# Kernel tuning notes

Measured on AMD Instinct MI355X. Metric: run time of the kernel, lower is better.

Reference implementation:

```python
import jax, jax.numpy as jnp
import numpy as np

N, M = 50000, 16
NODE_DIM, EDGE_DIM = 128, 64
CONCAT_DIM = 2 * NODE_DIM + EDGE_DIM  # 320
LN_EPS = 1e-6  # flax.linen.LayerNorm default


def setup_inputs() -> dict:
    key = jax.random.key(0)
    ks = jax.random.split(key, 5)
    x = jax.random.normal(ks[0], (N, NODE_DIM), dtype=jnp.float32)
    nbr_fea = jax.random.normal(ks[1], (N, M, EDGE_DIM), dtype=jnp.float32)
    nbr_fea_idx = jax.random.randint(ks[2], (N, M), 0, N)
    ln_scale = jnp.ones((NODE_DIM,), dtype=jnp.float32)
    ln_bias = jnp.zeros((NODE_DIM,), dtype=jnp.float32)
    # lecun_normal-ish init scaled by fan-in (flax Dense default is lecun_normal)
    W1 = jax.random.normal(ks[3], (CONCAT_DIM, NODE_DIM), dtype=jnp.float32) / np.sqrt(CONCAT_DIM)
    b1 = jnp.zeros((NODE_DIM,), dtype=jnp.float32)
    W2 = jax.random.normal(ks[4], (NODE_DIM, NODE_DIM), dtype=jnp.float32) / np.sqrt(NODE_DIM)
    b2 = jnp.zeros((NODE_DIM,), dtype=jnp.float32)
    return {"x": x, "nbr_fea": nbr_fea, "nbr_fea_idx": nbr_fea_idx,
            "ln_scale": ln_scale, "ln_bias": ln_bias,
            "W1": W1, "b1": b1, "W2": W2, "b2": b2}


def _layer_norm(x, scale, bias):
    mu = jnp.mean(x, axis=-1, keepdims=True)
    var = jnp.mean(jnp.square(x - mu), axis=-1, keepdims=True)
    return (x - mu) * jax.lax.rsqrt(var + LN_EPS) * scale + bias


def reference(x, nbr_fea, nbr_fea_idx, ln_scale, ln_bias, W1, b1, W2, b2):
    # x: [N, D], nbr_fea: [N, M, E], nbr_fea_idx: [N, M]
    x_normed = _layer_norm(x, ln_scale, ln_bias)                 # [N, D]
    x_nbr = jnp.take(x_normed, nbr_fea_idx, axis=0)              # [N, M, D]
    m = nbr_fea_idx.shape[1]
    x_center = jnp.broadcast_to(x_normed[:, None, :], (x.shape[0], m, x.shape[1]))
    concat = jnp.concatenate([x_center, x_nbr, nbr_fea], axis=-1)  # [N, M, 2D+E]
    h = jax.nn.silu(jnp.einsum('nmc,cd->nmd', concat, W1) + b1)   # [N, M, D]
    msg = jnp.einsum('nmd,de->nme', h, W2) + b2                   # [N, M, D]
    agg = jnp.sum(msg, axis=1)                                    # [N, D]
    return x + agg
```

## Files before the change

kernel.cpp:

```cpp
#include <hip/hip_runtime.h>
#include <math.h>

#define N_NODES 50000
#define M_NBR 16
#define D 128
#define E 64

typedef __attribute__((ext_vector_type(8))) __bf16 bf16x8;
typedef __attribute__((ext_vector_type(4))) float f32x4;

__device__ __forceinline__ void gload16(const void* g, void* l) {
  __builtin_amdgcn_global_load_lds(
      (const __attribute__((address_space(1))) void*)g,
      (__attribute__((address_space(3))) void*)l, 16, 0, 0);
}

__device__ __forceinline__ int swz(int o) { return o ^ (((o >> 7) & 7) << 4); }


__global__ __launch_bounds__(256) void k_prep(const float* __restrict__ W1,
                                              const float* __restrict__ W2,
                                              __bf16* __restrict__ w1a_f,
                                              __bf16* __restrict__ w1b_f,
                                              __bf16* __restrict__ w1c_f,
                                              __bf16* __restrict__ w2_f) {
  const int t = blockIdx.x * 256 + threadIdx.x;
  if (t < 16384) {
    const int j = t & 7, r = (t >> 3) & 15, c = (t >> 7) & 3, q = t >> 9;
    const int kt = q & 3, dt = q >> 2;
    w1a_f[t] = (__bf16)W1[(kt * 32 + c * 8 + j) * 128 + dt * 16 + r];
  } else if (t < 32768) {
    const int u = t - 16384;
    const int j = u & 7, r = (u >> 3) & 15, c = (u >> 7) & 3, q = u >> 9;
    const int kt = q & 3, dt = q >> 2;
    w1b_f[u] = (__bf16)W1[(128 + kt * 32 + c * 8 + j) * 128 + dt * 16 + r];
  } else if (t < 40960) {
    const int u = t - 32768;
    const int j = u & 7, r = (u >> 3) & 15, c = (u >> 7) & 3, q = u >> 9;
    const int kt = q & 1, dt = q >> 1;
    w1c_f[u] = (__bf16)W1[(256 + kt * 32 + c * 8 + j) * 128 + dt * 16 + r];
  } else if (t < 57344) {
    const int u = t - 40960;
    const int j = u & 7, r = (u >> 3) & 15, c = (u >> 7) & 3, q = u >> 9;
    const int kt = q & 3, dt = q >> 2;
    const int i = kt * 32 + c * 8 + j;
    const int ak = (i & 7) * 16 + (i >> 3);
    w2_f[u] = (__bf16)W2[ak * 128 + dt * 16 + r];
  }
}

__global__ __launch_bounds__(256) void k_t12f(const float* __restrict__ x,
                                              const float* __restrict__ sc,
                                              const float* __restrict__ bi,
                                              const __bf16* __restrict__ w1a_f,
                                              const __bf16* __restrict__ w1b_f,
                                              const float* __restrict__ b1,
                                              __bf16* __restrict__ t1bp,
                                              __bf16* __restrict__ t2bp) {
  const int wave = blockIdx.x * 4 + (threadIdx.x >> 6);
  if (wave >= N_NODES / 16) return;
  const int lane = threadIdx.x & 63;
  const int r = lane & 15, c = lane >> 4;
  const int node0 = wave * 16;

  const float* row = x + (size_t)(node0 + r) * 128 + c * 8;
  f32x4 va[8];
  #pragma unroll
  for (int kt = 0; kt < 4; ++kt) {
    va[2 * kt]     = *(const f32x4*)(row + kt * 32);
    va[2 * kt + 1] = *(const f32x4*)(row + kt * 32 + 4);
  }
  float s = 0.f;
  #pragma unroll
  for (int q = 0; q < 8; ++q) s += va[q][0] + va[q][1] + va[q][2] + va[q][3];
  s += __shfl_xor(s, 16, 64);
  s += __shfl_xor(s, 32, 64);
  const float mu = s * (1.0f / 128.0f);
  float qs = 0.f;
  #pragma unroll
  for (int q = 0; q < 8; ++q) {
    #pragma unroll
    for (int e = 0; e < 4; ++e) { const float dxx = va[q][e] - mu; qs += dxx * dxx; }
  }
  qs += __shfl_xor(qs, 16, 64);
  qs += __shfl_xor(qs, 32, 64);
  const float rs = rsqrtf(qs * (1.0f / 128.0f) + 1e-6f);

  bf16x8 af[4];
  #pragma unroll
  for (int kt = 0; kt < 4; ++kt) {
    const f32x4 s_lo = *(const f32x4*)(sc + kt * 32 + c * 8);
    const f32x4 s_hi = *(const f32x4*)(sc + kt * 32 + c * 8 + 4);
    const f32x4 b_lo = *(const f32x4*)(bi + kt * 32 + c * 8);
    const f32x4 b_hi = *(const f32x4*)(bi + kt * 32 + c * 8 + 4);
    #pragma unroll
    for (int e = 0; e < 4; ++e) {
      af[kt][e]     = (__bf16)(((va[2 * kt][e]     - mu) * rs) * s_lo[e] + b_lo[e]);
      af[kt][4 + e] = (__bf16)(((va[2 * kt + 1][e] - mu) * rs) * s_hi[e] + b_hi[e]);
    }
  }

  const bf16x8* wa = (const bf16x8*)w1a_f;
  const bf16x8* wb = (const bf16x8*)w1b_f;
  f32x4 acc1[8], acc2[8];
  #pragma unroll
  for (int dt = 0; dt < 8; ++dt) { acc1[dt] = (f32x4){0,0,0,0}; acc2[dt] = (f32x4){0,0,0,0}; }
  #pragma unroll
  for (int dt = 0; dt < 8; ++dt) {
    #pragma unroll
    for (int kt = 0; kt < 4; ++kt) {
      const bf16x8 bfa = wa[(dt * 4 + kt) * 64 + c * 16 + r];
      acc1[dt] = __builtin_amdgcn_mfma_f32_16x16x32_bf16(af[kt], bfa, acc1[dt], 0, 0, 0);
      const bf16x8 bfb = wb[(dt * 4 + kt) * 64 + c * 16 + r];
      acc2[dt] = __builtin_amdgcn_mfma_f32_16x16x32_bf16(af[kt], bfb, acc2[dt], 0, 0, 0);
    }
  }

  float b1v[8];
  #pragma unroll
  for (int dt = 0; dt < 8; ++dt) b1v[dt] = b1[dt * 16 + r];
  #pragma unroll
  for (int j = 0; j < 4; ++j) {
    const int node = node0 + c * 4 + j;
    bf16x8 t1v, t2v;
    #pragma unroll
    for (int dt = 0; dt < 8; ++dt) {
      t1v[dt] = (__bf16)(acc1[dt][j] + b1v[dt]);
      t2v[dt] = (__bf16)acc2[dt][j];
    }
    *(bf16x8*)(t1bp + (size_t)node * 128 + r * 8) = t1v;
    *(bf16x8*)(t2bp + (size_t)node * 128 + r * 8) = t2v;
  }
}

__global__ __launch_bounds__(256, 4) void k_edge(const float* __restrict__ nbr,
                                                 const int* __restrict__ idx,
                                                 const __bf16* __restrict__ t1bp,
                                                 const __bf16* __restrict__ t2bp,
                                                 const __bf16* __restrict__ w1c_f,
                                                 __bf16* __restrict__ hsum_b) {
  __shared__ __bf16 wlds[8192];
  const int lane = threadIdx.x & 63;
  const int wid  = threadIdx.x >> 6;
  const int r = lane & 15, c = lane >> 4;

  {
    const int s0 = wid * 1024 + lane * 16;
    #pragma unroll
    for (int q = 0; q < 4; ++q) {
      const int s = s0 + q * 4096;
      gload16((const char*)w1c_f + swz(s), (char*)wlds + s);
    }
  }

  const int n = blockIdx.x * 4 + wid;
  const int4 g = *(const int4*)(idx + n * M_NBR + c * 4);
  const float* arow = nbr + (size_t)n * (M_NBR * E) + r * E + c * 8;
  const f32x4 a0 = *(const f32x4*)(arow);
  const f32x4 a1 = *(const f32x4*)(arow + 4);
  const f32x4 a2 = *(const f32x4*)(arow + 32);
  const f32x4 a3 = *(const f32x4*)(arow + 36);
  const bf16x8 t1v = *(const bf16x8*)(t1bp + (size_t)n * 128 + r * 8);

  __syncthreads();

  const bf16x8 tg0 = *(const bf16x8*)(t2bp + (size_t)g.x * 128 + r * 8);
  const bf16x8 tg1 = *(const bf16x8*)(t2bp + (size_t)g.y * 128 + r * 8);
  const bf16x8 tg2 = *(const bf16x8*)(t2bp + (size_t)g.z * 128 + r * 8);
  const bf16x8 tg3 = *(const bf16x8*)(t2bp + (size_t)g.w * 128 + r * 8);

  bf16x8 af0, af1;
  #pragma unroll
  for (int e = 0; e < 4; ++e) {
    af0[e] = (__bf16)a0[e]; af0[4 + e] = (__bf16)a1[e];
    af1[e] = (__bf16)a2[e]; af1[4 + e] = (__bf16)a3[e];
  }

  f32x4 acc[8];
  #pragma unroll
  for (int dt = 0; dt < 8; ++dt) acc[dt] = (f32x4){0, 0, 0, 0};
  #pragma unroll
  for (int dt = 0; dt < 8; ++dt) {
    const int o0 = ((dt * 2 + 0) * 64 + c * 16 + r) * 16;
    const int o1 = ((dt * 2 + 1) * 64 + c * 16 + r) * 16;
    const bf16x8 b0 = *(const bf16x8*)((const char*)wlds + swz(o0));
    const bf16x8 b1 = *(const bf16x8*)((const char*)wlds + swz(o1));
    acc[dt] = __builtin_amdgcn_mfma_f32_16x16x32_bf16(af0, b0, acc[dt], 0, 0, 0);
    acc[dt] = __builtin_amdgcn_mfma_f32_16x16x32_bf16(af1, b1, acc[dt], 0, 0, 0);
  }

  float ssum[8];
  #pragma unroll
  for (int dt = 0; dt < 8; ++dt) {
    const float tb = (float)t1v[dt];
    float s = 0.f;
    { const float h = acc[dt][0] + tb + (float)tg0[dt]; s += __fdividef(h, 1.0f + __expf(-h)); }
    { const float h = acc[dt][1] + tb + (float)tg1[dt]; s += __fdividef(h, 1.0f + __expf(-h)); }
    { const float h = acc[dt][2] + tb + (float)tg2[dt]; s += __fdividef(h, 1.0f + __expf(-h)); }
    { const float h = acc[dt][3] + tb + (float)tg3[dt]; s += __fdividef(h, 1.0f + __expf(-h)); }
    s += __shfl_xor(s, 16, 64);
    s += __shfl_xor(s, 32, 64);
    ssum[dt] = s;
  }
  if (lane < 16) {
    bf16x8 hs;
    #pragma unroll
    for (int dt = 0; dt < 8; ++dt) hs[dt] = (__bf16)ssum[dt];
    *(bf16x8*)(hsum_b + (size_t)n * 128 + r * 8) = hs;
  }
}

__global__ __launch_bounds__(256) void k_out(const __bf16* __restrict__ hsum_b,
                                             const __bf16* __restrict__ w2_f,
                                             const float* __restrict__ b2,
                                             const float* __restrict__ x,
                                             float* __restrict__ out) {
  const int wave = blockIdx.x * 4 + (threadIdx.x >> 6);
  if (wave >= N_NODES / 16) return;
  const int lane = threadIdx.x & 63;
  const int r = lane & 15, c = lane >> 4;
  const int node0 = wave * 16;

  const __bf16* row = hsum_b + (size_t)(node0 + r) * 128 + c * 8;
  bf16x8 af[4];
  #pragma unroll
  for (int kt = 0; kt < 4; ++kt) af[kt] = *(const bf16x8*)(row + kt * 32);

  const bf16x8* w2 = (const bf16x8*)w2_f;
  f32x4 acc[8];
  #pragma unroll
  for (int dt = 0; dt < 8; ++dt) acc[dt] = (f32x4){0,0,0,0};
  #pragma unroll
  for (int dt = 0; dt < 8; ++dt) {
    #pragma unroll
    for (int kt = 0; kt < 4; ++kt) {
      const bf16x8 bf = w2[(dt * 4 + kt) * 64 + c * 16 + r];
      acc[dt] = __builtin_amdgcn_mfma_f32_16x16x32_bf16(af[kt], bf, acc[dt], 0, 0, 0);
    }
  }

  float b2v[8];
  #pragma unroll
  for (int dt = 0; dt < 8; ++dt) b2v[dt] = 16.0f * b2[dt * 16 + r];
  #pragma unroll
  for (int j = 0; j < 4; ++j) {
    const int node = node0 + c * 4 + j;
    #pragma unroll
    for (int dt = 0; dt < 8; ++dt) {
      const size_t o = (size_t)node * 128 + dt * 16 + r;
      out[o] = x[o] + acc[dt][j] + b2v[dt];
    }
  }
}

extern "C" void kernel_launch(void* const* d_in, const int* in_sizes, int n_in,
                              void* d_out, int out_size, void* d_ws, size_t ws_size,
                              hipStream_t stream) {
  const float* x        = (const float*)d_in[0];
  const float* nbr_fea  = (const float*)d_in[1];
  const int*   nbr_idx  = (const int*)d_in[2];
  const float* ln_scale = (const float*)d_in[3];
  const float* ln_bias  = (const float*)d_in[4];
  const float* W1       = (const float*)d_in[5];
  const float* b1       = (const float*)d_in[6];
  const float* W2       = (const float*)d_in[7];
  const float* b2       = (const float*)d_in[8];
  float* out = (float*)d_out;

  char* ws = (char*)d_ws;
  __bf16* t1bp   = (__bf16*)(ws);
  __bf16* hsum_b = (__bf16*)(ws + 12800000);
  __bf16* t2bp   = (__bf16*)(ws + 25600000);
  __bf16* w1a_f  = (__bf16*)(ws + 38400000);
  __bf16* w1b_f  = (__bf16*)(ws + 38433536);
  __bf16* w1c_f  = (__bf16*)(ws + 38466304);
  __bf16* w2_f   = (__bf16*)(ws + 38482688);

  k_prep <<<224, 256, 0, stream>>>(W1, W2, w1a_f, w1b_f, w1c_f, w2_f);
  k_t12f <<<(N_NODES / 16 + 3) / 4, 256, 0, stream>>>(x, ln_scale, ln_bias,
                                                      w1a_f, w1b_f, b1, t1bp, t2bp);
  k_edge <<<N_NODES / 4, 256, 0, stream>>>(nbr_fea, nbr_idx, t1bp, t2bp, w1c_f, hsum_b);
  k_out  <<<(N_NODES / 16 + 3) / 4, 256, 0, stream>>>(hsum_b, w2_f, b2, x, out);
}
```

Measured before the change: 122.7 us.

## Fuse edge aggregation and output projection into one kernel via LDS staging

Merges the edge kernel and the W2 output kernel. Each block now handles 16 nodes, four per wave, and stages the bf16 per-node silu sums in padded LDS, then runs the W2 MFMA and the residual add in the same block. This removes the hsum round trip through global memory and one kernel launch. The W2 prep permutation is changed to a plain row order to match the new LDS layout. In exchange, blocks are 4x fewer and each wave processes its nodes serially, which may reduce latency hiding for the gathered loads.

Measured after the change: 120.0 us. -2.2%, faster.

```diff
diff --git a/kernel.cpp b/kernel.cpp
--- a/kernel.cpp
+++ b/kernel.cpp
@@ -43,9 +43,7 @@
     const int u = t - 40960;
     const int j = u & 7, r = (u >> 3) & 15, c = (u >> 7) & 3, q = u >> 9;
     const int kt = q & 3, dt = q >> 2;
-    const int i = kt * 32 + c * 8 + j;
-    const int ak = (i & 7) * 16 + (i >> 3);
-    w2_f[u] = (__bf16)W2[ak * 128 + dt * 16 + r];
+    w2_f[u] = (__bf16)W2[(kt * 32 + c * 8 + j) * 128 + dt * 16 + r];
   }
 }
 
@@ -133,16 +131,23 @@
   }
 }
 
-__global__ __launch_bounds__(256, 4) void k_edge(const float* __restrict__ nbr,
-                                                 const int* __restrict__ idx,
-                                                 const __bf16* __restrict__ t1bp,
-                                                 const __bf16* __restrict__ t2bp,
-                                                 const __bf16* __restrict__ w1c_f,
-                                                 __bf16* __restrict__ hsum_b) {
+#define HPITCH 136
+
+__global__ __launch_bounds__(256, 4) void k_edge2(const float* __restrict__ nbr,
+                                                  const int* __restrict__ idx,
+                                                  const __bf16* __restrict__ t1bp,
+                                                  const __bf16* __restrict__ t2bp,
+                                                  const __bf16* __restrict__ w1c_f,
+                                                  const __bf16* __restrict__ w2_f,
+                                                  const float* __restrict__ b2,
+                                                  const float* __restrict__ x,
+                                                  float* __restrict__ out) {
   __shared__ __bf16 wlds[8192];
+  __shared__ __bf16 hlds[16 * HPITCH];
   const int lane = threadIdx.x & 63;
   const int wid  = threadIdx.x >> 6;
   const int r = lane & 15, c = lane >> 4;
+  const int nb0 = blockIdx.x * 16;
 
   {
     const int s0 = wid * 1024 + lane * 16;
@@ -152,104 +157,89 @@
       gload16((const char*)w1c_f + swz(s), (char*)wlds + s);
     }
   }
-
-  const int n = blockIdx.x * 4 + wid;
-  const int4 g = *(const int4*)(idx + n * M_NBR + c * 4);
-  const float* arow = nbr + (size_t)n * (M_NBR * E) + r * E + c * 8;
-  const f32x4 a0 = *(const f32x4*)(arow);
-  const f32x4 a1 = *(const f32x4*)(arow + 4);
-  const f32x4 a2 = *(const f32x4*)(arow + 32);
-  const f32x4 a3 = *(const f32x4*)(arow + 36);
-  const bf16x8 t1v = *(const bf16x8*)(t1bp + (size_t)n * 128 + r * 8);
-
   __syncthreads();
 
-  const bf16x8 tg0 = *(const bf16x8*)(t2bp + (size_t)g.x * 128 + r * 8);
-  const bf16x8 tg1 = *(const bf16x8*)(t2bp + (size_t)g.y * 128 + r * 8);
-  const bf16x8 tg2 = *(const bf16x8*)(t2bp + (size_t)g.z * 128 + r * 8);
-  const bf16x8 tg3 = *(const bf16x8*)(t2bp + (size_t)g.w * 128 + r * 8);
-
-  bf16x8 af0, af1;
-  #pragma unroll
-  for (int e = 0; e < 4; ++e) {
-    af0[e] = (__bf16)a0[e]; af0[4 + e] = (__bf16)a1[e];
-    af1[e] = (__bf16)a2[e]; af1[4 + e] = (__bf16)a3[e];
-  }
-
-  f32x4 acc[8];
-  #pragma unroll
-  for (int dt = 0; dt < 8; ++dt) acc[dt] = (f32x4){0, 0, 0, 0};
-  #pragma unroll
-  for (int dt = 0; dt < 8; ++dt) {
-    const int o0 = ((dt * 2 + 0) * 64 + c * 16 + r) * 16;
-    const int o1 = ((dt * 2 + 1) * 64 + c * 16 + r) * 16;
-    const bf16x8 b0 = *(const bf16x8*)((const char*)wlds + swz(o0));
-    const bf16x8 b1 = *(const bf16x8*)((const char*)wlds + swz(o1));
-    acc[dt] = __builtin_amdgcn_mfma_f32_16x16x32_bf16(af0, b0, acc[dt], 0, 0, 0);
-    acc[dt] = __builtin_amdgcn_mfma_f32_16x16x32_bf16(af1, b1, acc[dt], 0, 0, 0);
-  }
-
-  float ssum[8];
-  #pragma unroll
-  for (int dt = 0; dt < 8; ++dt) {
-    const float tb = (float)t1v[dt];
-    float s = 0.f;
-    { const float h = acc[dt][0] + tb + (float)tg0[dt]; s += __fdividef(h, 1.0f + __expf(-h)); }
-    { const float h = acc[dt][1] + tb + (float)tg1[dt]; s += __fdividef(h, 1.0f + __expf(-h)); }
-    { const float h = acc[dt][2] + tb + (float)tg2[dt]; s += __fdividef(h, 1.0f + __expf(-h)); }
-    { const float h = acc[dt][3] + tb + (float)tg3[dt]; s += __fdividef(h, 1.0f + __expf(-h)); }
-    s += __shfl_xor(s, 16, 64);
-    s += __shfl_xor(s, 32, 64);
-    ssum[dt] = s;
-  }
-  if (lane < 16) {
-    bf16x8 hs;
-    #pragma unroll
-    for (int dt = 0; dt < 8; ++dt) hs[dt] = (__bf16)ssum[dt];
-    *(bf16x8*)(hsum_b + (size_t)n * 128 + r * 8) = hs;
-  }
-}
-
-__global__ __launch_bounds__(256) void k_out(const __bf16* __restrict__ hsum_b,
-                                             const __bf16* __restrict__ w2_f,
-                                             const float* __restrict__ b2,
-                                             const float* __restrict__ x,
-                                             float* __restrict__ out) {
-  const int wave = blockIdx.x * 4 + (threadIdx.x >> 6);
-  if (wave >= N_NODES / 16) return;
-  const int lane = threadIdx.x & 63;
-  const int r = lane & 15, c = lane >> 4;
-  const int node0 = wave * 16;
-
-  const __bf16* row = hsum_b + (size_t)(node0 + r) * 128 + c * 8;
-  bf16x8 af[4];
-  #pragma unroll
-  for (int kt = 0; kt < 4; ++kt) af[kt] = *(const bf16x8*)(row + kt * 32);
-
+  #pragma unroll
+  for (int i = 0; i < 4; ++i) {
+    const int row = wid * 4 + i;
+    const int n = nb0 + row;
+
+    const int4 g = *(const int4*)(idx + n * M_NBR + c * 4);
+    const float* arow = nbr + (size_t)n * (M_NBR * E) + r * E + c * 8;
+    const f32x4 a0 = *(const f32x4*)(arow);
+    const f32x4 a1 = *(const f32x4*)(arow + 4);
+    const f32x4 a2 = *(const f32x4*)(arow + 32);
+    const f32x4 a3 = *(const f32x4*)(arow + 36);
+    const bf16x8 t1v = *(const bf16x8*)(t1bp + (size_t)n * 128 + r * 8);
+    const bf16x8 tg0 = *(const bf16x8*)(t2bp + (size_t)g.x * 128 + r * 8);
+    const bf16x8 tg1 = *(const bf16x8*)(t2bp + (size_t)g.y * 128 + r * 8);
+    const bf16x8 tg2 = *(const bf16x8*)(t2bp + (size_t)g.z * 128 + r * 8);
+    const bf16x8 tg3 = *(const bf16x8*)(t2bp + (size_t)g.w * 128 + r * 8);
+
+    bf16x8 af0, af1;
+    #pragma unroll
+    for (int e = 0; e < 4; ++e) {
+      af0[e] = (__bf16)a0[e]; af0[4 + e] = (__bf16)a1[e];
+      af1[e] = (__bf16)a2[e]; af1[4 + e] = (__bf16)a3[e];
+    }
+
+    f32x4 acc[8];
+    #pragma unroll
+    for (int dt = 0; dt < 8; ++dt) acc[dt] = (f32x4){0, 0, 0, 0};
+    #pragma unroll
+    for (int dt = 0; dt < 8; ++dt) {
+      const int o0 = ((dt * 2 + 0) * 64 + c * 16 + r) * 16;
+      const int o1 = ((dt * 2 + 1) * 64 + c * 16 + r) * 16;
+      const bf16x8 b0 = *(const bf16x8*)((const char*)wlds + swz(o0));
+      const bf16x8 b1 = *(const bf16x8*)((const char*)wlds + swz(o1));
+      acc[dt] = __builtin_amdgcn_mfma_f32_16x16x32_bf16(af0, b0, acc[dt], 0, 0, 0);
+      acc[dt] = __builtin_amdgcn_mfma_f32_16x16x32_bf16(af1, b1, acc[dt], 0, 0, 0);
+    }
+
+    #pragma unroll
+    for (int dt = 0; dt < 8; ++dt) {
+      const float tb = (float)t1v[dt];
+      float s = 0.f;
+      { const float h = acc[dt][0] + tb + (float)tg0[dt]; s += __fdividef(h, 1.0f + __expf(-h)); }
+      { const float h = acc[dt][1] + tb + (float)tg1[dt]; s += __fdividef(h, 1.0f + __expf(-h)); }
+      { const float h = acc[dt][2] + tb + (float)tg2[dt]; s += __fdividef(h, 1.0f + __expf(-h)); }
+      { const float h = acc[dt][3] + tb + (float)tg3[dt]; s += __fdividef(h, 1.0f + __expf(-h)); }
+      s += __shfl_xor(s, 16, 64);
+      s += __shfl_xor(s, 32, 64);
+      if (lane < 16) hlds[row * HPITCH + dt * 16 + lane] = (__bf16)s;
+    }
+  }
+  __syncthreads();
+
+  const int dtA = wid * 2, dtB = wid * 2 + 1;
   const bf16x8* w2 = (const bf16x8*)w2_f;
-  f32x4 acc[8];
-  #pragma unroll
-  for (int dt = 0; dt < 8; ++dt) acc[dt] = (f32x4){0,0,0,0};
-  #pragma unroll
-  for (int dt = 0; dt < 8; ++dt) {
-    #pragma unroll
-    for (int kt = 0; kt < 4; ++kt) {
-      const bf16x8 bf = w2[(dt * 4 + kt) * 64 + c * 16 + r];
-      acc[dt] = __builtin_amdgcn_mfma_f32_16x16x32_bf16(af[kt], bf, acc[dt], 0, 0, 0);
-    }
-  }
-
-  float b2v[8];
-  #pragma unroll
-  for (int dt = 0; dt < 8; ++dt) b2v[dt] = 16.0f * b2[dt * 16 + r];
+  bf16x8 bA[4], bB[4];
+  #pragma unroll
+  for (int kt = 0; kt < 4; ++kt) {
+    bA[kt] = w2[(dtA * 4 + kt) * 64 + c * 16 + r];
+    bB[kt] = w2[(dtB * 4 + kt) * 64 + c * 16 + r];
+  }
+  bf16x8 haf[4];
+  #pragma unroll
+  for (int kt = 0; kt < 4; ++kt)
+    haf[kt] = *(const bf16x8*)(hlds + r * HPITCH + kt * 32 + c * 8);
+
+  f32x4 accA = (f32x4){0,0,0,0}, accB = (f32x4){0,0,0,0};
+  #pragma unroll
+  for (int kt = 0; kt < 4; ++kt) {
+    accA = __builtin_amdgcn_mfma_f32_16x16x32_bf16(haf[kt], bA[kt], accA, 0, 0, 0);
+    accB = __builtin_amdgcn_mfma_f32_16x16x32_bf16(haf[kt], bB[kt], accB, 0, 0, 0);
+  }
+
+  const float b2A = 16.0f * b2[dtA * 16 + r];
+  const float b2B = 16.0f * b2[dtB * 16 + r];
   #pragma unroll
   for (int j = 0; j < 4; ++j) {
-    const int node = node0 + c * 4 + j;
-    #pragma unroll
-    for (int dt = 0; dt < 8; ++dt) {
-      const size_t o = (size_t)node * 128 + dt * 16 + r;
-      out[o] = x[o] + acc[dt][j] + b2v[dt];
-    }
+    const int node = nb0 + c * 4 + j;
+    const size_t oA = (size_t)node * 128 + dtA * 16 + r;
+    const size_t oB = (size_t)node * 128 + dtB * 16 + r;
+    out[oA] = x[oA] + accA[j] + b2A;
+    out[oB] = x[oB] + accB[j] + b2B;
   }
 }
 
@@ -269,16 +259,15 @@
 
   char* ws = (char*)d_ws;
   __bf16* t1bp   = (__bf16*)(ws);
-  __bf16* hsum_b = (__bf16*)(ws + 12800000);
-  __bf16* t2bp   = (__bf16*)(ws + 25600000);
-  __bf16* w1a_f  = (__bf16*)(ws + 38400000);
-  __bf16* w1b_f  = (__bf16*)(ws + 38433536);
-  __bf16* w1c_f  = (__bf16*)(ws + 38466304);
-  __bf16* w2_f   = (__bf16*)(ws + 38482688);
-
-  k_prep <<<224, 256, 0, stream>>>(W1, W2, w1a_f, w1b_f, w1c_f, w2_f);
-  k_t12f <<<(N_NODES / 16 + 3) / 4, 256, 0, stream>>>(x, ln_scale, ln_bias,
-                                                      w1a_f, w1b_f, b1, t1bp, t2bp);
-  k_edge <<<N_NODES / 4, 256, 0, stream>>>(nbr_fea, nbr_idx, t1bp, t2bp, w1c_f, hsum_b);
-  k_out  <<<(N_NODES / 16 + 3) / 4, 256, 0, stream>>>(hsum_b, w2_f, b2, x, out);
-}
+  __bf16* t2bp   = (__bf16*)(ws + 12800000);
+  __bf16* w1a_f  = (__bf16*)(ws + 25600000);
+  __bf16* w1b_f  = (__bf16*)(ws + 25632768);
+  __bf16* w1c_f  = (__bf16*)(ws + 25665536);
+  __bf16* w2_f   = (__bf16*)(ws + 25681920);
+
+  k_prep  <<<224, 256, 0, stream>>>(W1, W2, w1a_f, w1b_f, w1c_f, w2_f);
+  k_t12f  <<<(N_NODES / 16 + 3) / 4, 256, 0, stream>>>(x, ln_scale, ln_bias,
+                                                       w1a_f, w1b_f, b1, t1bp, t2bp);
+  k_edge2 <<<N_NODES / 16, 256, 0, stream>>>(nbr_fea, nbr_idx, t1bp, t2bp,
+                                             w1c_f, w2_f, b2, x, out);
+}
```

## Restructure edge kernel with a dedicated gather wave staging neighbor rows in LDS

Applied to the files above, without the earlier changes.

Replaces the one-node-per-wave edge kernel with a 192-thread block of 8 nodes. One wave issues async global-to-LDS loads for the gathered t2 rows (XOR-swizzled) and the t1 rows, while the two compute waves load the W1c weights and their streaming neighbor features, then each handle four nodes. The aim is to spread each block's weight load over more nodes and to move the random gathers onto async LDS loads. In exchange it leaves a third of the threads idle after the barrier, uses more LDS and caps occupancy at 2 blocks per unit.

After: 153.8 us. 25.3% more time.

```diff
diff --git a/kernel.cpp b/kernel.cpp
--- a/kernel.cpp
+++ b/kernel.cpp
@@ -133,49 +133,29 @@
   }
 }
 
-__global__ __launch_bounds__(256, 4) void k_edge(const float* __restrict__ nbr,
-                                                 const int* __restrict__ idx,
-                                                 const __bf16* __restrict__ t1bp,
-                                                 const __bf16* __restrict__ t2bp,
-                                                 const __bf16* __restrict__ w1c_f,
-                                                 __bf16* __restrict__ hsum_b) {
-  __shared__ __bf16 wlds[8192];
-  const int lane = threadIdx.x & 63;
-  const int wid  = threadIdx.x >> 6;
-  const int r = lane & 15, c = lane >> 4;
-
-  {
-    const int s0 = wid * 1024 + lane * 16;
-    #pragma unroll
-    for (int q = 0; q < 4; ++q) {
-      const int s = s0 + q * 4096;
-      gload16((const char*)w1c_f + swz(s), (char*)wlds + s);
-    }
-  }
-
-  const int n = blockIdx.x * 4 + wid;
-  const int4 g = *(const int4*)(idx + n * M_NBR + c * 4);
+struct SA { f32x4 a0, a1, a2, a3; };
+
+__device__ __forceinline__ SA load_stream(const float* __restrict__ nbr,
+                                          int n, int r, int c) {
+  SA v;
   const float* arow = nbr + (size_t)n * (M_NBR * E) + r * E + c * 8;
-  const f32x4 a0 = *(const f32x4*)(arow);
-  const f32x4 a1 = *(const f32x4*)(arow + 4);
-  const f32x4 a2 = *(const f32x4*)(arow + 32);
-  const f32x4 a3 = *(const f32x4*)(arow + 36);
-  const bf16x8 t1v = *(const bf16x8*)(t1bp + (size_t)n * 128 + r * 8);
-
-  __syncthreads();
-
-  const bf16x8 tg0 = *(const bf16x8*)(t2bp + (size_t)g.x * 128 + r * 8);
-  const bf16x8 tg1 = *(const bf16x8*)(t2bp + (size_t)g.y * 128 + r * 8);
-  const bf16x8 tg2 = *(const bf16x8*)(t2bp + (size_t)g.z * 128 + r * 8);
-  const bf16x8 tg3 = *(const bf16x8*)(t2bp + (size_t)g.w * 128 + r * 8);
-
+  v.a0 = *(const f32x4*)(arow);
+  v.a1 = *(const f32x4*)(arow + 4);
+  v.a2 = *(const f32x4*)(arow + 32);
+  v.a3 = *(const f32x4*)(arow + 36);
+  return v;
+}
+
+__device__ __forceinline__ void compute_node(const SA& v, const __bf16* wlds,
+                                             const __bf16* tgl, const __bf16* t1l,
+                                             int slot, int n, int lane, int r, int c,
+                                             __bf16* __restrict__ hsum_b) {
   bf16x8 af0, af1;
   #pragma unroll
   for (int e = 0; e < 4; ++e) {
-    af0[e] = (__bf16)a0[e]; af0[4 + e] = (__bf16)a1[e];
-    af1[e] = (__bf16)a2[e]; af1[4 + e] = (__bf16)a3[e];
-  }
-
+    af0[e] = (__bf16)v.a0[e]; af0[4 + e] = (__bf16)v.a1[e];
+    af1[e] = (__bf16)v.a2[e]; af1[4 + e] = (__bf16)v.a3[e];
+  }
   f32x4 acc[8];
   #pragma unroll
   for (int dt = 0; dt < 8; ++dt) acc[dt] = (f32x4){0, 0, 0, 0};
@@ -188,6 +168,11 @@
     acc[dt] = __builtin_amdgcn_mfma_f32_16x16x32_bf16(af0, b0, acc[dt], 0, 0, 0);
     acc[dt] = __builtin_amdgcn_mfma_f32_16x16x32_bf16(af1, b1, acc[dt], 0, 0, 0);
   }
+  const bf16x8 tg0 = *(const bf16x8*)((const char*)tgl + slot * 4096 + (c * 4 + 0) * 256 + ((r ^ ((c * 4 + 0) & 7)) * 16));
+  const bf16x8 tg1 = *(const bf16x8*)((const char*)tgl + slot * 4096 + (c * 4 + 1) * 256 + ((r ^ ((c * 4 + 1) & 7)) * 16));
+  const bf16x8 tg2 = *(const bf16x8*)((const char*)tgl + slot * 4096 + (c * 4 + 2) * 256 + ((r ^ ((c * 4 + 2) & 7)) * 16));
+  const bf16x8 tg3 = *(const bf16x8*)((const char*)tgl + slot * 4096 + (c * 4 + 3) * 256 + ((r ^ ((c * 4 + 3) & 7)) * 16));
+  const bf16x8 t1v = *(const bf16x8*)((const char*)t1l + slot * 256 + r * 16);
 
   float ssum[8];
   #pragma unroll
@@ -208,6 +193,64 @@
     for (int dt = 0; dt < 8; ++dt) hs[dt] = (__bf16)ssum[dt];
     *(bf16x8*)(hsum_b + (size_t)n * 128 + r * 8) = hs;
   }
+}
+
+__global__ __launch_bounds__(192, 2) void k_edge3(const float* __restrict__ nbr,
+                                                  const int* __restrict__ idx,
+                                                  const __bf16* __restrict__ t1bp,
+                                                  const __bf16* __restrict__ t2bp,
+                                                  const __bf16* __restrict__ w1c_f,
+                                                  __bf16* __restrict__ hsum_b) {
+  __shared__ __bf16 wlds[8192];
+  __shared__ __bf16 tgl[8 * 2048];
+  __shared__ __bf16 t1l[8 * 128];
+  const int lane = threadIdx.x & 63;
+  const int wid  = threadIdx.x >> 6;
+  const int r = lane & 15, c = lane >> 4;
+  const int nb0 = blockIdx.x * 8;
+
+  SA s0, s1, s2, s3;
+  if (wid == 2) {
+    {
+      const int v0 = lane >> 4;
+      gload16((const char*)t1bp + ((size_t)(nb0 + v0) * 128 + r * 8) * 2,
+              (char*)t1l);
+      const int v1 = 4 + (lane >> 4);
+      gload16((const char*)t1bp + ((size_t)(nb0 + v1) * 128 + r * 8) * 2,
+              (char*)t1l + 1024);
+    }
+    #pragma unroll
+    for (int v = 0; v < 8; ++v) {
+      #pragma unroll
+      for (int k = 0; k < 4; ++k) {
+        const int rho = k * 4 + (lane >> 4);
+        const int g = idx[(nb0 + v) * M_NBR + rho];
+        const int rs = (lane & 15) ^ (rho & 7);
+        gload16((const char*)t2bp + ((size_t)g * 128 + rs * 8) * 2,
+                (char*)tgl + v * 4096 + k * 1024);
+      }
+    }
+  } else {
+    #pragma unroll
+    for (int q = 0; q < 8; ++q) {
+      const int chunk = wid * 8 + q;
+      const int s = chunk * 1024 + lane * 16;
+      gload16((const char*)w1c_f + swz(s), (char*)wlds + chunk * 1024);
+    }
+    s0 = load_stream(nbr, nb0 + wid * 4 + 0, r, c);
+    s1 = load_stream(nbr, nb0 + wid * 4 + 1, r, c);
+    s2 = load_stream(nbr, nb0 + wid * 4 + 2, r, c);
+    s3 = load_stream(nbr, nb0 + wid * 4 + 3, r, c);
+  }
+
+  __syncthreads();
+  if (wid == 2) return;
+
+  const int slot0 = wid * 4;
+  compute_node(s0, wlds, tgl, t1l, slot0 + 0, nb0 + slot0 + 0, lane, r, c, hsum_b);
+  compute_node(s1, wlds, tgl, t1l, slot0 + 1, nb0 + slot0 + 1, lane, r, c, hsum_b);
+  compute_node(s2, wlds, tgl, t1l, slot0 + 2, nb0 + slot0 + 2, lane, r, c, hsum_b);
+  compute_node(s3, wlds, tgl, t1l, slot0 + 3, nb0 + slot0 + 3, lane, r, c, hsum_b);
 }
 
 __global__ __launch_bounds__(256) void k_out(const __bf16* __restrict__ hsum_b,
@@ -269,16 +312,17 @@
 
   char* ws = (char*)d_ws;
   __bf16* t1bp   = (__bf16*)(ws);
-  __bf16* hsum_b = (__bf16*)(ws + 12800000);
-  __bf16* t2bp   = (__bf16*)(ws + 25600000);
+  __bf16* t2bp   = (__bf16*)(ws + 12800000);
+  __bf16* hsum_b = (__bf16*)(ws + 25600000);
   __bf16* w1a_f  = (__bf16*)(ws + 38400000);
-  __bf16* w1b_f  = (__bf16*)(ws + 38433536);
-  __bf16* w1c_f  = (__bf16*)(ws + 38466304);
-  __bf16* w2_f   = (__bf16*)(ws + 38482688);
-
-  k_prep <<<224, 256, 0, stream>>>(W1, W2, w1a_f, w1b_f, w1c_f, w2_f);
-  k_t12f <<<(N_NODES / 16 + 3) / 4, 256, 0, stream>>>(x, ln_scale, ln_bias,
-                                                      w1a_f, w1b_f, b1, t1bp, t2bp);
-  k_edge <<<N_NODES / 4, 256, 0, stream>>>(nbr_fea, nbr_idx, t1bp, t2bp, w1c_f, hsum_b);
-  k_out  <<<(N_NODES / 16 + 3) / 4, 256, 0, stream>>>(hsum_b, w2_f, b2, x, out);
-}
+  __bf16* w1b_f  = (__bf16*)(ws + 38432768);
+  __bf16* w1c_f  = (__bf16*)(ws + 38465536);
+  __bf16* w2_f   = (__bf16*)(ws + 38481920);
+
+  k_prep  <<<224, 256, 0, stream>>>(W1, W2, w1a_f, w1b_f, w1c_f, w2_f);
+  k_t12f  <<<(N_NODES / 16 + 3) / 4, 256, 0, stream>>>(x, ln_scale, ln_bias,
+                                                       w1a_f, w1b_f, b1, t1bp, t2bp);
+  k_edge3 <<<N_NODES / 8, 192, 0, stream>>>(nbr_fea, nbr_idx, t1bp, t2bp,
+                                            w1c_f, hsum_b);
+  k_out   <<<(N_NODES / 16 + 3) / 4, 256, 0, stream>>>(hsum_b, w2_f, b2, x, out);
+}
```
